# Kernel optimization log

Measured on AMD Instinct MI355X. Metric: run time of the kernel, lower is better.

The kernel has to match this reference:

```python
import jax, jax.numpy as jnp
import numpy as np

BATCH = 65536
SEQ_LEN = 1024  # matrix_size**2
DEGREE = 7


def chebvander(t, deg):
    """Chebyshev Vandermonde matrix: T_0..T_deg evaluated at t. Returns [..., deg+1]."""
    cols = [jnp.ones_like(t), t]
    for _ in range(2, deg + 1):
        cols.append(2.0 * t * cols[-1] - cols[-2])
    return jnp.stack(cols[: deg + 1], axis=-1)


def setup_inputs() -> dict:
    key = jax.random.key(0)
    x = jax.random.normal(key, (BATCH, SEQ_LEN), dtype=jnp.float32)
    # strictly increasing time grid over the natural Chebyshev domain [-1, 1]
    time_grid = jnp.linspace(-1.0, 1.0, SEQ_LEN, dtype=jnp.float32)
    return {"x": x, "time_grid": time_grid}


def reference(x, time_grid):
    B, L = x.shape
    M = int(np.sqrt(L))          # matrix_size (32)
    # values[b, i, j] = x[b, i + j*M]  -> reshape to (M_j, M_i) then transpose
    values = x.reshape(B, M, M).transpose(0, 2, 1)          # [B, i, j]
    times = time_grid.reshape(M, M).T                        # [i, j]
    # Chebyshev least-squares fit per row i (same times for every batch element):
    V = chebvander(times, DEGREE)                            # [i, j, D]
    G = jnp.einsum('ijd,ije->ide', V, V)                     # [M, D, D] Gram matrices
    rhs = jnp.einsum('ijd,bij->bid', V, values)              # [B, M, D]
    # normal-equation solve == lstsq solution for well-conditioned Vandermonde
    coeffs = jnp.linalg.solve(G[None], rhs[..., None])[..., 0]  # [B, M, D]
    return coeffs
```

## Files before the change

kernel.cpp:

```cpp
#include <hip/hip_runtime.h>

#define MM 32
#define DD 8
#define LL 1024
#define NBATCH 65536
#define NBLK 2048
#define RPB (NBATCH / NBLK)
#define RPP 4
#define NPH (RPB / RPP)

__device__ float g_Wt[MM * DD * MM];

__global__ void precompute_w_kernel(const float* __restrict__ tg) {
    const int i = blockIdx.x;
    const int t = threadIdx.x;

    __shared__ float  V[MM][DD];
    __shared__ double A[DD][2 * DD];

    if (t < MM) {
        float tt = tg[t * MM + i];
        float c0 = 1.0f, c1 = tt;
        V[t][0] = c0;
        V[t][1] = c1;
        for (int e = 2; e < DD; ++e) {
            float c2 = 2.0f * tt * c1 - c0;
            V[t][e] = c2;
            c0 = c1; c1 = c2;
        }
    }
    __syncthreads();

    {
        int d = t >> 3, e = t & 7;
        double s = 0.0;
        for (int j = 0; j < MM; ++j) s += (double)V[j][d] * (double)V[j][e];
        A[d][e] = s;
        A[d][DD + e] = (d == e) ? 1.0 : 0.0;
    }
    __syncthreads();

    if (t == 0) {
        for (int p = 0; p < DD; ++p) {
            double inv = 1.0 / A[p][p];
            for (int c = p; c < 2 * DD; ++c) A[p][c] *= inv;
            for (int r2 = 0; r2 < DD; ++r2) {
                if (r2 == p) continue;
                double f = A[r2][p];
                for (int c = p; c < 2 * DD; ++c) A[r2][c] -= f * A[p][c];
            }
        }
    }
    __syncthreads();

    for (int k = t; k < DD * MM; k += 64) {
        int d = k >> 5;
        int j = k & 31;
        double s = 0.0;
        for (int e = 0; e < DD; ++e) s += A[d][DD + e] * (double)V[j][e];
        g_Wt[(i * DD + d) * MM + j] = (float)s;
    }
}

__global__ __launch_bounds__(256, 4) void poly_apply_kernel(
        const float* __restrict__ x,
        float* __restrict__ out) {
    __shared__ float xl[2][RPP][1156];

    const int t = threadIdx.x;
    const int i = t >> 3;

    float w[32];
    {
        const float4* wp = (const float4*)g_Wt + t * 8;
#pragma unroll
        for (int q = 0; q < 8; ++q) {
            float4 v4 = wp[q];
            w[4 * q + 0] = v4.x;
            w[4 * q + 1] = v4.y;
            w[4 * q + 2] = v4.z;
            w[4 * q + 3] = v4.w;
        }
    }

    const int r0 = blockIdx.x * RPB;
    const int staddr = 4 * t + 4 * (t >> 3);
    const float4* xr = (const float4*)(x + (size_t)r0 * LL) + t;

    float4 v[RPP];

#pragma unroll
    for (int q = 0; q < RPP; ++q) v[q] = xr[q * 256];
#pragma unroll
    for (int q = 0; q < RPP; ++q) *(float4*)&xl[0][q][staddr] = v[q];
#pragma unroll
    for (int q = 0; q < RPP; ++q) v[q] = xr[(RPP + q) * 256];
    __syncthreads();

    for (int ph = 0; ph < NPH; ++ph) {
        const int p = ph & 1;

        if (ph + 1 < NPH) {
#pragma unroll
            for (int q = 0; q < RPP; ++q) *(float4*)&xl[p ^ 1][q][staddr] = v[q];
        }
        if (ph + 2 < NPH) {
#pragma unroll
            for (int q = 0; q < RPP; ++q)
                v[q] = xr[(size_t)((ph + 2) * RPP + q) * 256];
        }

#pragma unroll
        for (int rr = 0; rr < RPP; ++rr) {
            const float* xb = &xl[p][rr][i];
            float acc = 0.f;
#pragma unroll
            for (int j = 0; j < 32; ++j)
                acc = fmaf(w[j], xb[j * 36], acc);
            out[(size_t)(r0 + ph * RPP + rr) * 256 + t] = acc;
        }

        __syncthreads();
    }
}

extern "C" void kernel_launch(void* const* d_in, const int* in_sizes, int n_in,
                              void* d_out, int out_size, void* d_ws, size_t ws_size,
                              hipStream_t stream) {
    const float* x  = (const float*)d_in[0];
    const float* tg = (const float*)d_in[1];
    float* out = (float*)d_out;
    (void)d_ws; (void)ws_size;

    precompute_w_kernel<<<32, 64, 0, stream>>>(tg);
    poly_apply_kernel<<<NBLK, 256, 0, stream>>>(x, out);
}
```

Baseline: 428.8 us.

## Transpose rows in LDS and compute two outputs per thread with float4 reads

```diff
diff --git a/kernel.cpp b/kernel.cpp
--- a/kernel.cpp
+++ b/kernel.cpp
@@ -6,8 +6,7 @@
 #define NBATCH 65536
 #define NBLK 2048
 #define RPB (NBATCH / NBLK)
-#define RPP 4
-#define NPH (RPB / RPP)
+#define NPASS (RPB / 2)
 
 __device__ float g_Wt[MM * DD * MM];
 
@@ -65,59 +64,87 @@
 __global__ __launch_bounds__(256, 4) void poly_apply_kernel(
         const float* __restrict__ x,
         float* __restrict__ out) {
-    __shared__ float xl[2][RPP][1156];
+    __shared__ __align__(16) float xT[2][2][1152];
 
-    const int t = threadIdx.x;
-    const int i = t >> 3;
+    const int t   = threadIdx.x;
+    const int rs  = t >> 7;
+    const int tt  = t & 127;
+    const int si  = tt & 31;
+    const int sq  = tt >> 5;
+    const int ci  = tt >> 2;
+    const int dp  = t & 3;
 
-    float w[32];
+    float w0[32], w1[32];
     {
-        const float4* wp = (const float4*)g_Wt + t * 8;
+        const float4* wp = (const float4*)g_Wt + (ci * DD + 2 * dp) * 8;
 #pragma unroll
         for (int q = 0; q < 8; ++q) {
-            float4 v4 = wp[q];
-            w[4 * q + 0] = v4.x;
-            w[4 * q + 1] = v4.y;
-            w[4 * q + 2] = v4.z;
-            w[4 * q + 3] = v4.w;
+            float4 a = wp[q];
+            w0[4 * q + 0] = a.x; w0[4 * q + 1] = a.y;
+            w0[4 * q + 2] = a.z; w0[4 * q + 3] = a.w;
+            float4 b = wp[q + 8];
+            w1[4 * q + 0] = b.x; w1[4 * q + 1] = b.y;
+            w1[4 * q + 2] = b.z; w1[4 * q + 3] = b.w;
         }
+    }
+#pragma unroll
+    for (int j = 0; j < 32; ++j) {
+        asm volatile("" : "+v"(w0[j]));
+        asm volatile("" : "+v"(w1[j]));
     }
 
     const int r0 = blockIdx.x * RPB;
-    const int staddr = 4 * t + 4 * (t >> 3);
-    const float4* xr = (const float4*)(x + (size_t)r0 * LL) + t;
+    const float* xbase = x + (size_t)(r0 + rs) * LL + si + 256 * sq;
+    const int wboff = si * 36 + 8 * sq;
 
-    float4 v[RPP];
+    float v[8];
 
 #pragma unroll
-    for (int q = 0; q < RPP; ++q) v[q] = xr[q * 256];
+    for (int c = 0; c < 8; ++c) v[c] = xbase[32 * c];
+    {
+        float* wb = &xT[0][rs][wboff];
 #pragma unroll
-    for (int q = 0; q < RPP; ++q) *(float4*)&xl[0][q][staddr] = v[q];
+        for (int k = 0; k < 4; ++k) {
+            float2 p2; p2.x = v[2 * k]; p2.y = v[2 * k + 1];
+            *(float2*)&wb[2 * k] = p2;
+        }
+    }
 #pragma unroll
-    for (int q = 0; q < RPP; ++q) v[q] = xr[(RPP + q) * 256];
+    for (int c = 0; c < 8; ++c) v[c] = xbase[2 * LL + 32 * c];
     __syncthreads();
 
-    for (int ph = 0; ph < NPH; ++ph) {
-        const int p = ph & 1;
-
-        if (ph + 1 < NPH) {
+    for (int p = 0; p < NPASS; ++p) {
+        if (p + 1 < NPASS) {
+            float* wb = &xT[(p + 1) & 1][rs][wboff];
 #pragma unroll
-            for (int q = 0; q < RPP; ++q) *(float4*)&xl[p ^ 1][q][staddr] = v[q];
+            for (int k = 0; k < 4; ++k) {
+                float2 p2; p2.x = v[2 * k]; p2.y = v[2 * k + 1];
+                *(float2*)&wb[2 * k] = p2;
+            }
         }
-        if (ph + 2 < NPH) {
+        if (p + 2 < NPASS) {
 #pragma unroll
-            for (int q = 0; q < RPP; ++q)
-                v[q] = xr[(size_t)((ph + 2) * RPP + q) * 256];
+            for (int c = 0; c < 8; ++c)
+                v[c] = xbase[(size_t)(p + 2) * 2 * LL + 32 * c];
         }
 
+        {
+            const float* xb = &xT[p & 1][rs][ci * 36];
+            float a0 = 0.f, a1 = 0.f;
 #pragma unroll
-        for (int rr = 0; rr < RPP; ++rr) {
-            const float* xb = &xl[p][rr][i];
-            float acc = 0.f;
-#pragma unroll
-            for (int j = 0; j < 32; ++j)
-                acc = fmaf(w[j], xb[j * 36], acc);
-            out[(size_t)(r0 + ph * RPP + rr) * 256 + t] = acc;
+            for (int m = 0; m < 8; ++m) {
+                float4 xq = *(const float4*)&xb[4 * m];
+                a0 = fmaf(w0[4 * m + 0], xq.x, a0);
+                a1 = fmaf(w1[4 * m + 0], xq.x, a1);
+                a0 = fmaf(w0[4 * m + 1], xq.y, a0);
+                a1 = fmaf(w1[4 * m + 1], xq.y, a1);
+                a0 = fmaf(w0[4 * m + 2], xq.z, a0);
+                a1 = fmaf(w1[4 * m + 2], xq.z, a1);
+                a0 = fmaf(w0[4 * m + 3], xq.w, a0);
+                a1 = fmaf(w1[4 * m + 3], xq.w, a1);
+            }
+            float2 o; o.x = a0; o.y = a1;
+            *(float2*)&out[(size_t)(r0 + 2 * p + rs) * 256 + ci * 8 + 2 * dp] = o;
         }
 
         __syncthreads();
```

After: 397.1 us. 7.4% less time.
